# Kernel optimization log

Measured on AMD Instinct MI355X. Metric: run time of the kernel, lower is better.

Reference implementation:

```python
import jax, jax.numpy as jnp
import numpy as np

N = 50000   # nodes
E = 800000  # edges (avg degree 16)
F = 128     # feature dim (input = hidden = output)
H = 8       # heads
D = F // H  # head dim = 16
L = 4       # layers


def setup_inputs() -> dict:
    key = jax.random.key(0)
    ks = jax.random.split(key, 11)
    x = jax.random.normal(ks[0], (N, F), dtype=jnp.float32)
    edge_index = jax.random.randint(ks[1], (2, E), 0, N, dtype=jnp.int64)
    s = 1.0 / np.sqrt(F)
    Wq = jax.random.normal(ks[2], (L, F, F), dtype=jnp.float32) * s
    Wk = jax.random.normal(ks[3], (L, F, F), dtype=jnp.float32) * s
    Wv = jax.random.normal(ks[4], (L, F, F), dtype=jnp.float32) * s
    Ws = jax.random.normal(ks[5], (L, F, F), dtype=jnp.float32) * s  # lin_skip (root weight)
    bq = jax.random.normal(ks[6], (L, F), dtype=jnp.float32) * 0.02
    bk = jax.random.normal(ks[7], (L, F), dtype=jnp.float32) * 0.02
    bv = jax.random.normal(ks[8], (L, F), dtype=jnp.float32) * 0.02
    bs = jax.random.normal(ks[9], (L, F), dtype=jnp.float32) * 0.02
    return {"x": x, "edge_index": edge_index, "Wq": Wq, "bq": bq,
            "Wk": Wk, "bk": bk, "Wv": Wv, "bv": bv, "Ws": Ws, "bs": bs}


def _transformer_conv(x, src, dst, Wq, bq, Wk, bk, Wv, bv, Ws, bs):
    # Q from destination nodes, K/V from source nodes (PyG TransformerConv).
    q = (x @ Wq + bq)[dst].reshape(E, H, D)
    k = (x @ Wk + bk)[src].reshape(E, H, D)
    alpha = (q * k).sum(-1) * (1.0 / np.sqrt(D))            # [E, H]
    # segment softmax over edges grouped by destination node
    amax = jax.ops.segment_max(alpha, dst, num_segments=N)   # [N, H]
    amax = jnp.where(jnp.isfinite(amax), amax, 0.0)
    p = jnp.exp(alpha - amax[dst])
    denom = jax.ops.segment_sum(p, dst, num_segments=N)      # [N, H]
    a = p / denom[dst]                                       # [E, H]
    v = (x @ Wv + bv)[src].reshape(E, H, D)
    msg = (a[..., None] * v).reshape(E, F)
    out = jax.ops.segment_sum(msg, dst, num_segments=N)      # concat heads
    out = out + x @ Ws + bs                                  # root/skip connection
    return out, a


def reference(x, edge_index, Wq, bq, Wk, bk, Wv, bv, Ws, bs):
    src, dst = edge_index[0], edge_index[1]
    alphas = []
    h = x
    for i in range(L - 1):
        h, a = _transformer_conv(h, src, dst, Wq[i], bq[i], Wk[i], bk[i],
                                 Wv[i], bv[i], Ws[i], bs[i])
        h = jax.nn.gelu(h, approximate=False)
        alphas.append(a)
    h, a = _transformer_conv(h, src, dst, Wq[-1], bq[-1], Wk[-1], bk[-1],
                             Wv[-1], bv[-1], Ws[-1], bs[-1])
    alphas.append(a)
    return h, jnp.stack(alphas)  # [N, F], [L, E, H]
```

## Files before the change

### kernel.cpp

```cpp
#include <hip/hip_runtime.h>
#include <math.h>

#define F 128
#define HEADS 8

typedef __attribute__((ext_vector_type(8))) short short8;
typedef __attribute__((ext_vector_type(4))) float floatx4;
typedef __attribute__((ext_vector_type(2))) _Float16 half2v;

__device__ __forceinline__ unsigned short f2bf(float f) {
    unsigned u = __float_as_uint(f);
    unsigned r = u + 0x7FFFu + ((u >> 16) & 1u);
    return (unsigned short)(r >> 16);
}

__device__ __forceinline__ half2v ashalf2(unsigned u) {
    return __builtin_bit_cast(half2v, u);
}
__device__ __forceinline__ unsigned pkh(float a, float b) {
    return __builtin_bit_cast(unsigned, __builtin_amdgcn_cvt_pkrtz(a, b));
}

#if __has_builtin(__builtin_amdgcn_fdot2)
#define FDOT2(a, b, c) __builtin_amdgcn_fdot2((a), (b), (c), false)
#else
#define FDOT2(a, b, c) ((c) + (float)(a)[0] * (float)(b)[0] + (float)(a)[1] * (float)(b)[1])
#endif


__global__ __launch_bounds__(256) void hist_k(const int* __restrict__ dst, int E, int* __restrict__ deg) {
    int e = blockIdx.x * 256 + threadIdx.x;
    if (e < E) atomicAdd(&deg[dst[e]], 1);
}

__global__ __launch_bounds__(256) void scan1_k(const int* __restrict__ deg, int N,
                                               int* __restrict__ start, int* __restrict__ partials) {
    __shared__ int sm[256];
    int t = threadIdx.x;
    int i = blockIdx.x * 256 + t;
    int v = (i < N) ? deg[i] : 0;
    sm[t] = v;
    __syncthreads();
    for (int off = 1; off < 256; off <<= 1) {
        int add = (t >= off) ? sm[t - off] : 0;
        __syncthreads();
        sm[t] += add;
        __syncthreads();
    }
    if (i < N) start[i] = sm[t] - v;
    if (t == 255) partials[blockIdx.x] = sm[t];
}

__global__ __launch_bounds__(256) void scan2_k(int* __restrict__ partials, int nb,
                                               int* __restrict__ start, int N, int E) {
    __shared__ int sm[256];
    int t = threadIdx.x;
    int v = (t < nb) ? partials[t] : 0;
    sm[t] = v;
    __syncthreads();
    for (int off = 1; off < 256; off <<= 1) {
        int add = (t >= off) ? sm[t - off] : 0;
        __syncthreads();
        sm[t] += add;
        __syncthreads();
    }
    if (t < nb) partials[t] = sm[t] - v;
    if (t == 0) start[N] = E;
}

__global__ __launch_bounds__(256) void scan3_k(int* __restrict__ start, int N, const int* __restrict__ partials) {
    int i = blockIdx.x * 256 + threadIdx.x;
    if (i < N) start[i] += partials[blockIdx.x];
}

__global__ __launch_bounds__(256) void fill_k(const int* __restrict__ src, const int* __restrict__ dst, int E,
                                              const int* __restrict__ start, int* __restrict__ cursor,
                                              int2* __restrict__ epair) {
    int e = blockIdx.x * 256 + threadIdx.x;
    if (e < E) {
        int dd = dst[e];
        int pos = atomicAdd(&cursor[dd], 1);
        epair[start[dd] + pos] = make_int2(e, src[e]);
    }
}

__global__ __launch_bounds__(256) void cvt_k(const float* __restrict__ x, unsigned short* __restrict__ xb, int total4) {
    int i = blockIdx.x * 256 + threadIdx.x;
    if (i < total4) {
        float4 v = ((const float4*)x)[i];
        ushort4 o;
        o.x = f2bf(v.x); o.y = f2bf(v.y); o.z = f2bf(v.z); o.w = f2bf(v.w);
        ((ushort4*)xb)[i] = o;
    }
}


__global__ __launch_bounds__(256) void wprep_k(
    const float* __restrict__ Wq, const float* __restrict__ Wk,
    const float* __restrict__ Wv, const float* __restrict__ Ws,
    unsigned short* __restrict__ out, int total) {
    int idx = blockIdx.x * 256 + threadIdx.x;
    if (idx >= total) return;
    int j = idx & 7;
    int lane = (idx >> 3) & 63;
    int rest = idx >> 9;
    int chunk = rest & 3;
    int ftile = (rest >> 2) & 7;
    int mat = (rest >> 5) & 3;
    int layer = rest >> 7;
    int k = chunk * 32 + (lane >> 4) * 8 + j;
    int f = ftile * 16 + (lane & 15);
    const float* W = (mat == 0) ? Wq : (mat == 1) ? Wk : (mat == 2) ? Wv : Ws;
    out[idx] = f2bf(W[((size_t)layer * F + k) * F + f]);
}


__global__ __launch_bounds__(256) void gemm_mfma(
    const unsigned short* __restrict__ xb, const unsigned short* __restrict__ wfrag,
    const float* __restrict__ bq, const float* __restrict__ bk,
    const float* __restrict__ bv, const float* __restrict__ bs,
    unsigned short* __restrict__ Qh, unsigned short* __restrict__ Kh,
    unsigned short* __restrict__ Vh, float* __restrict__ S, int N) {
    int wave = threadIdx.x >> 6;
    int lane = threadIdx.x & 63;
    int row0 = blockIdx.x * 32;
    int lm = lane & 15, quad = lane >> 4;
    const unsigned short* wf = wfrag + wave * 16384;

    floatx4 acc[2][8];
#pragma unroll
    for (int t = 0; t < 2; t++)
#pragma unroll
        for (int u = 0; u < 8; u++) acc[t][u] = (floatx4){0.f, 0.f, 0.f, 0.f};

#pragma unroll
    for (int chunk = 0; chunk < 4; chunk++) {
        short8 xfr[2];
#pragma unroll
        for (int t = 0; t < 2; t++) {
            int m = row0 + t * 16 + lm;
            m = (m < N) ? m : (N - 1);
            xfr[t] = *(const short8*)(xb + (size_t)m * F + chunk * 32 + quad * 8);
        }
#pragma unroll
        for (int u = 0; u < 8; u++) {
            short8 wfr = *(const short8*)(wf + ((u * 4 + chunk) * 64 + lane) * 8);
            acc[0][u] = __builtin_amdgcn_mfma_f32_16x16x32_bf16(wfr, xfr[0], acc[0][u], 0, 0, 0);
            acc[1][u] = __builtin_amdgcn_mfma_f32_16x16x32_bf16(wfr, xfr[1], acc[1][u], 0, 0, 0);
        }
    }

    const float* bias = (wave == 0) ? bq : (wave == 1) ? bk : (wave == 2) ? bv : bs;
#pragma unroll
    for (int u = 0; u < 8; u++) {
        float4 bv4 = *(const float4*)&bias[u * 16 + quad * 4];
#pragma unroll
        for (int t = 0; t < 2; t++) {
            int node = row0 + t * 16 + lm;
            if (node < N) {
                floatx4 a = acc[t][u];
                size_t off = (size_t)node * F + u * 16 + quad * 4;
                float v0 = a[0] + bv4.x, v1 = a[1] + bv4.y, v2 = a[2] + bv4.z, v3 = a[3] + bv4.w;
                if (wave == 3) {
                    *(float4*)&S[off] = make_float4(v0, v1, v2, v3);
                } else {
                    unsigned short* dp = (wave == 0) ? Qh : (wave == 1) ? Kh : Vh;
                    *(uint2*)&dp[off] = make_uint2(pkh(v0, v1), pkh(v2, v3));
                }
            }
        }
    }
}


__device__ __forceinline__ float gelu_exact(float v) {
    return 0.5f * v * (1.0f + erff(v * 0.70710678118654752f));
}

__global__ __launch_bounds__(256) void edge_k(
    const unsigned short* __restrict__ Qh, const unsigned short* __restrict__ Kh,
    const unsigned short* __restrict__ Vh, const float* __restrict__ S,
    const int* __restrict__ start, const int2* __restrict__ epair,
    float* __restrict__ aout,
    float* __restrict__ hout_f, unsigned short* __restrict__ hout_b,
    int N, int do_gelu) {
    __shared__ float wbuf[4][64][8];
    __shared__ int sbuf[4][64];
    __shared__ int ebuf[4][64];
    __shared__ float mdbuf[4][8];

    int wv = threadIdx.x >> 6;
    int lane = threadIdx.x & 63;
    int n = blockIdx.x * 4 + wv;
    if (n >= N) return;

    int beg = start[n], end = start[n + 1];
    int deg = end - beg;
    bool multi = deg > 64;
    int slot = lane >> 3, h = lane & 7;
    int g = lane >> 4, fl = lane & 15;
    int fh = fl >> 1;

    const unsigned short* qp = Qh + (size_t)n * F + h * 16;
    uint4 qa = *(const uint4*)(qp);
    uint4 qc = *(const uint4*)(qp + 8);
    half2v q0 = ashalf2(qa.x), q1 = ashalf2(qa.y), q2 = ashalf2(qa.z), q3 = ashalf2(qa.w);
    half2v q4 = ashalf2(qc.x), q5 = ashalf2(qc.y), q6 = ashalf2(qc.z), q7 = ashalf2(qc.w);

    float d = 0.f;
    float a0 = 0.f, a1 = 0.f, a2 = 0.f, a3 = 0.f, a4 = 0.f, a5 = 0.f, a6 = 0.f, a7 = 0.f;

    for (int c0 = beg; c0 < end; c0 += 64) {
        int cnt = min(64, end - c0);

        int nit = (cnt + 7) >> 3;
        for (int it = 0; it < nit; it++) {
            int idx = it * 8 + slot;
            bool val = idx < cnt;
            int gi = c0 + (val ? idx : 0);
            int2 pe = epair[gi];
            int s = pe.y;
            const unsigned short* kp = Kh + (size_t)s * F + h * 16;
            uint4 ka = *(const uint4*)(kp);
            uint4 kc = *(const uint4*)(kp + 8);
            float p0 = 0.f, p1 = 0.f;
            p0 = FDOT2(q0, ashalf2(ka.x), p0);
            p0 = FDOT2(q1, ashalf2(ka.y), p0);
            p0 = FDOT2(q2, ashalf2(ka.z), p0);
            p0 = FDOT2(q3, ashalf2(ka.w), p0);
            p1 = FDOT2(q4, ashalf2(kc.x), p1);
            p1 = FDOT2(q5, ashalf2(kc.y), p1);
            p1 = FDOT2(q6, ashalf2(kc.z), p1);
            p1 = FDOT2(q7, ashalf2(kc.w), p1);
            float w = __expf((p0 + p1) * 0.25f);
            if (!val) w = 0.f;
            d += w;
            wbuf[wv][idx][h] = w;
            if (h == 0) { sbuf[wv][idx] = s; ebuf[wv][idx] = pe.x; }
            if (multi && val) aout[(size_t)pe.x * HEADS + h] = w;
        }

        for (int j = 0; j < cnt; j += 8) {
            int idx0 = j + g;
            int idx1 = j + 4 + g;
            bool v0 = idx0 < cnt;
            bool v1 = idx1 < cnt;
            int s0 = sbuf[wv][v0 ? idx0 : 0];
            int s1 = sbuf[wv][v1 ? idx1 : 0];
            float w0 = wbuf[wv][v0 ? idx0 : 0][fh];
            float w1 = wbuf[wv][v1 ? idx1 : 0][fh];
            if (!v0) w0 = 0.f;
            if (!v1) w1 = 0.f;
            uint4 va = *(const uint4*)&Vh[(size_t)s0 * F + fl * 8];
            uint4 vb2 = *(const uint4*)&Vh[(size_t)s1 * F + fl * 8];
            half2v x0 = ashalf2(va.x), x1 = ashalf2(va.y), x2 = ashalf2(va.z), x3 = ashalf2(va.w);
            half2v y0 = ashalf2(vb2.x), y1 = ashalf2(vb2.y), y2 = ashalf2(vb2.z), y3 = ashalf2(vb2.w);
            a0 += w0 * (float)x0[0]; a1 += w0 * (float)x0[1];
            a2 += w0 * (float)x1[0]; a3 += w0 * (float)x1[1];
            a4 += w0 * (float)x2[0]; a5 += w0 * (float)x2[1];
            a6 += w0 * (float)x3[0]; a7 += w0 * (float)x3[1];
            a0 += w1 * (float)y0[0]; a1 += w1 * (float)y0[1];
            a2 += w1 * (float)y1[0]; a3 += w1 * (float)y1[1];
            a4 += w1 * (float)y2[0]; a5 += w1 * (float)y2[1];
            a6 += w1 * (float)y3[0]; a7 += w1 * (float)y3[1];
        }
    }

    d += __shfl_xor(d, 8);
    d += __shfl_xor(d, 16);
    d += __shfl_xor(d, 32);
    float inv_d = (d > 0.f) ? 1.f / d : 0.f;
    if (slot == 0) mdbuf[wv][h] = inv_d;

    if (!multi) {
        for (int idx = slot; idx < deg; idx += 8)
            aout[(size_t)ebuf[wv][idx] * HEADS + h] = wbuf[wv][idx][h] * inv_d;
    } else {
        for (int idx = slot; idx < deg; idx += 8)
            aout[(size_t)epair[beg + idx].x * HEADS + h] *= inv_d;
    }

    *(float4*)&wbuf[wv][lane][0] = make_float4(a0, a1, a2, a3);
    *(float4*)&wbuf[wv][lane][4] = make_float4(a4, a5, a6, a7);
    asm volatile("s_waitcnt lgkmcnt(0)" ::: "memory");

    int f0 = lane * 2;
    int frow = f0 >> 3;
    int fcol = f0 & 7;
    float t0 = 0.f, t1 = 0.f;
#pragma unroll
    for (int gg = 0; gg < 4; gg++) {
        float2 pr = *(const float2*)&wbuf[wv][gg * 16 + frow][fcol];
        t0 += pr.x; t1 += pr.y;
    }
    float invd = mdbuf[wv][lane >> 3];
    float2 sv = *(const float2*)&S[(size_t)n * F + f0];
    float o0 = t0 * invd + sv.x;
    float o1 = t1 * invd + sv.y;
    if (do_gelu) {
        o0 = gelu_exact(o0);
        o1 = gelu_exact(o1);
        unsigned ob = (unsigned)f2bf(o0) | ((unsigned)f2bf(o1) << 16);
        *(unsigned*)&hout_b[(size_t)n * F + f0] = ob;
    } else {
        *(float2*)&hout_f[(size_t)n * F + f0] = make_float2(o0, o1);
    }
}


extern "C" void kernel_launch(void* const* d_in, const int* in_sizes, int n_in,
                              void* d_out, int out_size, void* d_ws, size_t ws_size,
                              hipStream_t stream) {
    const float* x  = (const float*)d_in[0];
    const int*   ei = (const int*)d_in[1];
    const float* Wq = (const float*)d_in[2];
    const float* bq = (const float*)d_in[3];
    const float* Wk = (const float*)d_in[4];
    const float* bk = (const float*)d_in[5];
    const float* Wv = (const float*)d_in[6];
    const float* bv = (const float*)d_in[7];
    const float* Ws = (const float*)d_in[8];
    const float* bs = (const float*)d_in[9];

    const int N = in_sizes[0] / F;
    const int E = in_sizes[1] / 2;
    const int L = in_sizes[2] / (F * F);

    float* Sb = (float*)d_ws;
    unsigned short* Qh = (unsigned short*)(Sb + (size_t)N * F);
    unsigned short* xb = Qh + (size_t)N * F;
    unsigned short* hb = xb + (size_t)N * F;
    unsigned short* Kb = hb + (size_t)N * F;
    unsigned short* Vb = Kb + (size_t)N * F;
    unsigned short* wfrag = Vb + (size_t)N * F;
    int2* epair = (int2*)(wfrag + (size_t)L * 4 * 16384);
    int* start = (int*)(epair + E);
    int* cursor = start + (N + 1);
    int* partials = cursor + N;

    float* out_h = (float*)d_out;
    float* out_a = out_h + (size_t)N * F;

    const int* srcIdx = ei;
    const int* dstIdx = ei + E;

    int nbScan = (N + 255) / 256;
    hipMemsetAsync(cursor, 0, sizeof(int) * N, stream);
    hist_k<<<(E + 255) / 256, 256, 0, stream>>>(dstIdx, E, cursor);
    scan1_k<<<nbScan, 256, 0, stream>>>(cursor, N, start, partials);
    scan2_k<<<1, 256, 0, stream>>>(partials, nbScan, start, N, E);
    scan3_k<<<nbScan, 256, 0, stream>>>(start, N, partials);
    hipMemsetAsync(cursor, 0, sizeof(int) * N, stream);
    fill_k<<<(E + 255) / 256, 256, 0, stream>>>(srcIdx, dstIdx, E, start, cursor, epair);

    int wtotal = L * 4 * 16384;
    wprep_k<<<(wtotal + 255) / 256, 256, 0, stream>>>(Wq, Wk, Wv, Ws, wfrag, wtotal);
    cvt_k<<<((N * F / 4) + 255) / 256, 256, 0, stream>>>(x, xb, N * F / 4);

    for (int l = 0; l < L; ++l) {
        const unsigned short* hin = (l == 0) ? xb : hb;
        gemm_mfma<<<(N + 31) / 32, 256, 0, stream>>>(
            hin, wfrag + (size_t)l * 4 * 16384,
            bq + (size_t)l * F, bk + (size_t)l * F,
            bv + (size_t)l * F, bs + (size_t)l * F,
            Qh, Kb, Vb, Sb, N);
        edge_k<<<(N + 3) / 4, 256, 0, stream>>>(
            Qh, Kb, Vb, Sb, start, epair,
            out_a + (size_t)l * E * HEADS, out_h, hb, N, (l < L - 1) ? 1 : 0);
    }
}
```

Before: 679.6 us.

## Fuse setup kernels, merge scan passes, store skip in fp16, prefetch edge indices

Merges the bf16 conversion of x, the weight-fragment prep and the counter zeroing into one setup kernel, replacing two memsets and two launches. Folds the scan2 and scan3 passes into a single one-block kernel. Stores the skip projection S as fp16 instead of fp32, halving its write and read traffic at some precision cost. In edge_k, each 64-edge chunk's edge pairs are loaded once per lane into shared memory as byte offsets, instead of re-reading epair inside the inner loop.

```diff
diff --git a/kernel.cpp b/kernel.cpp
--- a/kernel.cpp
+++ b/kernel.cpp
@@ -26,6 +26,41 @@
 #else
 #define FDOT2(a, b, c) ((c) + (float)(a)[0] * (float)(b)[0] + (float)(a)[1] * (float)(b)[1])
 #endif
+
+
+__global__ __launch_bounds__(256) void setup_k(
+    const float* __restrict__ x, unsigned short* __restrict__ xb, int total4,
+    const float* __restrict__ Wq, const float* __restrict__ Wk,
+    const float* __restrict__ Wv, const float* __restrict__ Ws,
+    unsigned short* __restrict__ wfrag, int wtotal,
+    int* __restrict__ deg, int* __restrict__ cursor, int N) {
+    int idx = blockIdx.x * 256 + threadIdx.x;
+    if (idx < total4) {
+        float4 v = ((const float4*)x)[idx];
+        ushort4 o;
+        o.x = f2bf(v.x); o.y = f2bf(v.y); o.z = f2bf(v.z); o.w = f2bf(v.w);
+        ((ushort4*)xb)[idx] = o;
+        return;
+    }
+    idx -= total4;
+    if (idx < wtotal) {
+        int j = idx & 7;
+        int lane = (idx >> 3) & 63;
+        int rest = idx >> 9;
+        int chunk = rest & 3;
+        int ftile = (rest >> 2) & 7;
+        int mat = (rest >> 5) & 3;
+        int layer = rest >> 7;
+        int k = chunk * 32 + (lane >> 4) * 8 + j;
+        int f = ftile * 16 + (lane & 15);
+        const float* W = (mat == 0) ? Wq : (mat == 1) ? Wk : (mat == 2) ? Wv : Ws;
+        wfrag[idx] = f2bf(W[((size_t)layer * F + k) * F + f]);
+        return;
+    }
+    idx -= wtotal;
+    if (idx < N) deg[idx] = 0;
+    else if (idx < 2 * N) cursor[idx - N] = 0;
+}
 
 
 __global__ __launch_bounds__(256) void hist_k(const int* __restrict__ dst, int E, int* __restrict__ deg) {
@@ -51,8 +86,8 @@
     if (t == 255) partials[blockIdx.x] = sm[t];
 }
 
-__global__ __launch_bounds__(256) void scan2_k(int* __restrict__ partials, int nb,
-                                               int* __restrict__ start, int N, int E) {
+__global__ __launch_bounds__(256) void scan23_k(const int* __restrict__ partials, int nb,
+                                                int* __restrict__ start, int N, int E) {
     __shared__ int sm[256];
     int t = threadIdx.x;
     int v = (t < nb) ? partials[t] : 0;
@@ -64,13 +99,12 @@
         sm[t] += add;
         __syncthreads();
     }
-    if (t < nb) partials[t] = sm[t] - v;
+    int myoff = sm[t] - v;
+    __syncthreads();
+    sm[t] = myoff;
+    __syncthreads();
+    for (int i = t; i < N; i += 256) start[i] += sm[i >> 8];
     if (t == 0) start[N] = E;
-}
-
-__global__ __launch_bounds__(256) void scan3_k(int* __restrict__ start, int N, const int* __restrict__ partials) {
-    int i = blockIdx.x * 256 + threadIdx.x;
-    if (i < N) start[i] += partials[blockIdx.x];
 }
 
 __global__ __launch_bounds__(256) void fill_k(const int* __restrict__ src, const int* __restrict__ dst, int E,
@@ -84,43 +118,13 @@
     }
 }
 
-__global__ __launch_bounds__(256) void cvt_k(const float* __restrict__ x, unsigned short* __restrict__ xb, int total4) {
-    int i = blockIdx.x * 256 + threadIdx.x;
-    if (i < total4) {
-        float4 v = ((const float4*)x)[i];
-        ushort4 o;
-        o.x = f2bf(v.x); o.y = f2bf(v.y); o.z = f2bf(v.z); o.w = f2bf(v.w);
-        ((ushort4*)xb)[i] = o;
-    }
-}
-
-
-__global__ __launch_bounds__(256) void wprep_k(
-    const float* __restrict__ Wq, const float* __restrict__ Wk,
-    const float* __restrict__ Wv, const float* __restrict__ Ws,
-    unsigned short* __restrict__ out, int total) {
-    int idx = blockIdx.x * 256 + threadIdx.x;
-    if (idx >= total) return;
-    int j = idx & 7;
-    int lane = (idx >> 3) & 63;
-    int rest = idx >> 9;
-    int chunk = rest & 3;
-    int ftile = (rest >> 2) & 7;
-    int mat = (rest >> 5) & 3;
-    int layer = rest >> 7;
-    int k = chunk * 32 + (lane >> 4) * 8 + j;
-    int f = ftile * 16 + (lane & 15);
-    const float* W = (mat == 0) ? Wq : (mat == 1) ? Wk : (mat == 2) ? Wv : Ws;
-    out[idx] = f2bf(W[((size_t)layer * F + k) * F + f]);
-}
-
 
 __global__ __launch_bounds__(256) void gemm_mfma(
     const unsigned short* __restrict__ xb, const unsigned short* __restrict__ wfrag,
     const float* __restrict__ bq, const float* __restrict__ bk,
     const float* __restrict__ bv, const float* __restrict__ bs,
     unsigned short* __restrict__ Qh, unsigned short* __restrict__ Kh,
-    unsigned short* __restrict__ Vh, float* __restrict__ S, int N) {
+    unsigned short* __restrict__ Vh, unsigned short* __restrict__ Sh, int N) {
     int wave = threadIdx.x >> 6;
     int lane = threadIdx.x & 63;
     int row0 = blockIdx.x * 32;
@@ -151,6 +155,7 @@
     }
 
     const float* bias = (wave == 0) ? bq : (wave == 1) ? bk : (wave == 2) ? bv : bs;
+    unsigned short* dp = (wave == 0) ? Qh : (wave == 1) ? Kh : (wave == 2) ? Vh : Sh;
 #pragma unroll
     for (int u = 0; u < 8; u++) {
         float4 bv4 = *(const float4*)&bias[u * 16 + quad * 4];
@@ -160,13 +165,8 @@
             if (node < N) {
                 floatx4 a = acc[t][u];
                 size_t off = (size_t)node * F + u * 16 + quad * 4;
-                float v0 = a[0] + bv4.x, v1 = a[1] + bv4.y, v2 = a[2] + bv4.z, v3 = a[3] + bv4.w;
-                if (wave == 3) {
-                    *(float4*)&S[off] = make_float4(v0, v1, v2, v3);
-                } else {
-                    unsigned short* dp = (wave == 0) ? Qh : (wave == 1) ? Kh : Vh;
-                    *(uint2*)&dp[off] = make_uint2(pkh(v0, v1), pkh(v2, v3));
-                }
+                *(uint2*)&dp[off] = make_uint2(pkh(a[0] + bv4.x, a[1] + bv4.y),
+                                               pkh(a[2] + bv4.z, a[3] + bv4.w));
             }
         }
     }
@@ -179,7 +179,7 @@
 
 __global__ __launch_bounds__(256) void edge_k(
     const unsigned short* __restrict__ Qh, const unsigned short* __restrict__ Kh,
-    const unsigned short* __restrict__ Vh, const float* __restrict__ S,
+    const unsigned short* __restrict__ Vh, const unsigned short* __restrict__ Sh,
     const int* __restrict__ start, const int2* __restrict__ epair,
     float* __restrict__ aout,
     float* __restrict__ hout_f, unsigned short* __restrict__ hout_b,
@@ -213,14 +213,16 @@
     for (int c0 = beg; c0 < end; c0 += 64) {
         int cnt = min(64, end - c0);
 
+        int2 pe = epair[c0 + min(lane, cnt - 1)];
+        sbuf[wv][lane] = pe.y << 8;
+        ebuf[wv][lane] = pe.x;
+
         int nit = (cnt + 7) >> 3;
         for (int it = 0; it < nit; it++) {
             int idx = it * 8 + slot;
             bool val = idx < cnt;
-            int gi = c0 + (val ? idx : 0);
-            int2 pe = epair[gi];
-            int s = pe.y;
-            const unsigned short* kp = Kh + (size_t)s * F + h * 16;
+            int ofs = sbuf[wv][val ? idx : 0];
+            const unsigned short* kp = (const unsigned short*)((const char*)Kh + ofs) + h * 16;
             uint4 ka = *(const uint4*)(kp);
             uint4 kc = *(const uint4*)(kp + 8);
             float p0 = 0.f, p1 = 0.f;
@@ -236,8 +238,7 @@
             if (!val) w = 0.f;
             d += w;
             wbuf[wv][idx][h] = w;
-            if (h == 0) { sbuf[wv][idx] = s; ebuf[wv][idx] = pe.x; }
-            if (multi && val) aout[(size_t)pe.x * HEADS + h] = w;
+            if (multi && val) aout[(size_t)ebuf[wv][idx] * HEADS + h] = w;
         }
 
         for (int j = 0; j < cnt; j += 8) {
@@ -245,14 +246,14 @@
             int idx1 = j + 4 + g;
             bool v0 = idx0 < cnt;
             bool v1 = idx1 < cnt;
-            int s0 = sbuf[wv][v0 ? idx0 : 0];
-            int s1 = sbuf[wv][v1 ? idx1 : 0];
+            int o0s = sbuf[wv][v0 ? idx0 : 0];
+            int o1s = sbuf[wv][v1 ? idx1 : 0];
             float w0 = wbuf[wv][v0 ? idx0 : 0][fh];
             float w1 = wbuf[wv][v1 ? idx1 : 0][fh];
             if (!v0) w0 = 0.f;
             if (!v1) w1 = 0.f;
-            uint4 va = *(const uint4*)&Vh[(size_t)s0 * F + fl * 8];
-            uint4 vb2 = *(const uint4*)&Vh[(size_t)s1 * F + fl * 8];
+            uint4 va = *(const uint4*)((const char*)Vh + o0s + fl * 16);
+            uint4 vb2 = *(const uint4*)((const char*)Vh + o1s + fl * 16);
             half2v x0 = ashalf2(va.x), x1 = ashalf2(va.y), x2 = ashalf2(va.z), x3 = ashalf2(va.w);
             half2v y0 = ashalf2(vb2.x), y1 = ashalf2(vb2.y), y2 = ashalf2(vb2.z), y3 = ashalf2(vb2.w);
             a0 += w0 * (float)x0[0]; a1 += w0 * (float)x0[1];
@@ -294,9 +295,9 @@
         t0 += pr.x; t1 += pr.y;
     }
     float invd = mdbuf[wv][lane >> 3];
-    float2 sv = *(const float2*)&S[(size_t)n * F + f0];
-    float o0 = t0 * invd + sv.x;
-    float o1 = t1 * invd + sv.y;
+    half2v s2 = ashalf2(*(const unsigned*)&Sh[(size_t)n * F + f0]);
+    float o0 = t0 * invd + (float)s2[0];
+    float o1 = t1 * invd + (float)s2[1];
     if (do_gelu) {
         o0 = gelu_exact(o0);
         o1 = gelu_exact(o1);
@@ -326,8 +327,8 @@
     const int E = in_sizes[1] / 2;
     const int L = in_sizes[2] / (F * F);
 
-    float* Sb = (float*)d_ws;
-    unsigned short* Qh = (unsigned short*)(Sb + (size_t)N * F);
+    unsigned short* Sh = (unsigned short*)d_ws;
+    unsigned short* Qh = Sh + (size_t)N * F;
     unsigned short* xb = Qh + (size_t)N * F;
     unsigned short* hb = xb + (size_t)N * F;
     unsigned short* Kb = hb + (size_t)N * F;
@@ -336,7 +337,8 @@
     int2* epair = (int2*)(wfrag + (size_t)L * 4 * 16384);
     int* start = (int*)(epair + E);
     int* cursor = start + (N + 1);
-    int* partials = cursor + N;
+    int* deg = cursor + N;
+    int* partials = deg + N;
 
     float* out_h = (float*)d_out;
     float* out_a = out_h + (size_t)N * F;
@@ -344,18 +346,17 @@
     const int* srcIdx = ei;
     const int* dstIdx = ei + E;
 
+    int total4 = N * F / 4;
+    int wtotal = L * 4 * 16384;
+    int stotal = total4 + wtotal + 2 * N;
+    setup_k<<<(stotal + 255) / 256, 256, 0, stream>>>(
+        x, xb, total4, Wq, Wk, Wv, Ws, wfrag, wtotal, deg, cursor, N);
+
     int nbScan = (N + 255) / 256;
-    hipMemsetAsync(cursor, 0, sizeof(int) * N, stream);
-    hist_k<<<(E + 255) / 256, 256, 0, stream>>>(dstIdx, E, cursor);
-    scan1_k<<<nbScan, 256, 0, stream>>>(cursor, N, start, partials);
-    scan2_k<<<1, 256, 0, stream>>>(partials, nbScan, start, N, E);
-    scan3_k<<<nbScan, 256, 0, stream>>>(start, N, partials);
-    hipMemsetAsync(cursor, 0, sizeof(int) * N, stream);
+    hist_k<<<(E + 255) / 256, 256, 0, stream>>>(dstIdx, E, deg);
+    scan1_k<<<nbScan, 256, 0, stream>>>(deg, N, start, partials);
+    scan23_k<<<1, 256, 0, stream>>>(partials, nbScan, start, N, E);
     fill_k<<<(E + 255) / 256, 256, 0, stream>>>(srcIdx, dstIdx, E, start, cursor, epair);
-
-    int wtotal = L * 4 * 16384;
-    wprep_k<<<(wtotal + 255) / 256, 256, 0, stream>>>(Wq, Wk, Wv, Ws, wfrag, wtotal);
-    cvt_k<<<((N * F / 4) + 255) / 256, 256, 0, stream>>>(x, xb, N * F / 4);
 
     for (int l = 0; l < L; ++l) {
         const unsigned short* hin = (l == 0) ? xb : hb;
@@ -363,9 +364,9 @@
             hin, wfrag + (size_t)l * 4 * 16384,
             bq + (size_t)l * F, bk + (size_t)l * F,
             bv + (size_t)l * F, bs + (size_t)l * F,
-            Qh, Kb, Vb, Sb, N);
+            Qh, Kb, Vb, Sh, N);
         edge_k<<<(N + 3) / 4, 256, 0, stream>>>(
-            Qh, Kb, Vb, Sb, start, epair,
+            Qh, Kb, Vb, Sh, start, epair,
             out_a + (size_t)l * E * HEADS, out_h, hb, N, (l < L - 1) ? 1 : 0);
     }
 }
```

Result: no change. 668.1 us (-1.7%).
